# Kernel tuning notes

Hardware: AMD Instinct MI355X
Metric: run time of the kernel (lower is better)

## Reference

```python
import jax, jax.numpy as jnp
import numpy as np
from jax import lax

D_MODEL = 1024
D_IN = 1024        # expand=1 -> d_inner = d_model
N_STATE = 16       # d_state
DT_RANK = 64       # ceil(d_model/16)
D_FFN = 4096
BATCH, SEQ = 2, 2048


def setup_inputs() -> dict:
    key = jax.random.key(0)
    ks = jax.random.split(key, 12)
    r = lambda i, shape, s=0.02: jax.random.normal(ks[i], shape, jnp.float32) * s
    ones = lambda n: jnp.ones((n,), jnp.float32)
    zeros = lambda n: jnp.zeros((n,), jnp.float32)
    # S4D-real init for A
    A_log = jnp.log(jnp.tile(jnp.arange(1, N_STATE + 1, dtype=jnp.float32), (D_IN, 1)))
    return {
        "src": jax.random.normal(ks[0], (BATCH, SEQ, D_MODEL), jnp.float32),
        "in_proj_w": r(1, (2 * D_IN, D_MODEL)),
        "conv_w": r(2, (D_IN, 2), 0.5),
        "conv_b": zeros(D_IN),
        "x_proj_w": r(3, (DT_RANK + 2 * N_STATE, D_IN)),
        "dt_proj_w": r(4, (D_IN, DT_RANK), 0.1),
        "dt_proj_b": r(5, (D_IN,), 0.1),
        "A_log": A_log,
        "Dp": ones(D_IN),
        "out_proj_w": r(6, (D_MODEL, D_IN)),
        "mnorm_g": ones(D_MODEL), "mnorm_b": zeros(D_MODEL),
        "n1_g": ones(D_MODEL), "n1_b": zeros(D_MODEL),
        "n2_g": ones(D_MODEL), "n2_b": zeros(D_MODEL),
        "n3_g": ones(D_MODEL), "n3_b": zeros(D_MODEL),
        "ffn_w1": r(7, (D_FFN, D_MODEL)),
        "ffn_w2": r(8, (D_MODEL, D_FFN)),
        "fe_w": r(9, (D_MODEL, D_MODEL)),
        "fe_b": zeros(D_MODEL),
    }


def _ln(x, g, b, eps=1e-5):
    m = x.mean(-1, keepdims=True)
    v = ((x - m) ** 2).mean(-1, keepdims=True)
    return (x - m) / jnp.sqrt(v + eps) * g + b


def _mamba(x, in_proj_w, conv_w, conv_b, x_proj_w, dt_proj_w, dt_proj_b,
           A_log, Dp, out_proj_w):
    B, L, _ = x.shape
    xz = x @ in_proj_w.T                       # (B,L,2*D_IN)
    x_in, z = jnp.split(xz, 2, axis=-1)
    # depthwise causal conv1d, kernel size 2: y[l] = w0*x[l-1] + w1*x[l] + b
    x_prev = jnp.pad(x_in, ((0, 0), (1, 0), (0, 0)))[:, :L]
    x_c = jax.nn.silu(x_prev * conv_w[:, 0] + x_in * conv_w[:, 1] + conv_b)
    x_dbl = x_c @ x_proj_w.T                   # (B,L,DT_RANK+2N)
    dt, Bm, Cm = jnp.split(x_dbl, [DT_RANK, DT_RANK + N_STATE], axis=-1)
    delta = jax.nn.softplus(dt @ dt_proj_w.T + dt_proj_b)   # (B,L,D_IN)
    A = -jnp.exp(A_log)                        # (D_IN,N)
    deltaA = jnp.exp(delta[..., None] * A)                   # (B,L,D_IN,N)
    dBu = delta[..., None] * Bm[:, :, None, :] * x_c[..., None]

    def step(h, t):
        dA_t, dBu_t, C_t = t                   # (B,D_IN,N),(B,D_IN,N),(B,N)
        h = dA_t * h + dBu_t
        y = jnp.einsum('bdn,bn->bd', h, C_t)
        return h, y

    h0 = jnp.zeros((B, D_IN, N_STATE), x.dtype)
    _, ys = lax.scan(step, h0,
                     (deltaA.transpose(1, 0, 2, 3),
                      dBu.transpose(1, 0, 2, 3),
                      Cm.transpose(1, 0, 2)))
    y = ys.transpose(1, 0, 2)                  # (B,L,D_IN)
    y = (y + x_c * Dp) * jax.nn.silu(z)
    return y @ out_proj_w.T


def reference(src, in_proj_w, conv_w, conv_b, x_proj_w, dt_proj_w, dt_proj_b,
              A_log, Dp, out_proj_w, mnorm_g, mnorm_b, n1_g, n1_b, n2_g, n2_b,
              n3_g, n3_b, ffn_w1, ffn_w2, fe_w, fe_b):
    # src1 = MambaBlock(norm1(src)); dropout = identity (eval)
    h = _mamba(_ln(src, n1_g, n1_b), in_proj_w, conv_w, conv_b, x_proj_w,
               dt_proj_w, dt_proj_b, A_log, Dp, out_proj_w)
    src = src + _ln(h, mnorm_g, mnorm_b)
    # FFN: Linear -> LeakyReLU(0.01) -> Linear (no bias)
    f = _ln(src, n2_g, n2_b) @ ffn_w1.T
    f = jnp.where(f >= 0, f, 0.01 * f) @ ffn_w2.T
    src = src + f
    src = src + (_ln(src, n3_g, n3_b) @ fe_w.T + fe_b)
    return src
```

## Files before the change

### kernel.cpp

```cpp
#include <hip/hip_runtime.h>
#include <hip/hip_bf16.h>
#include <cstddef>

#define L_SEQ   2048
#define NBATCH  2
#define NROWS   (NBATCH * L_SEQ)
#define NSTATE  16
#define CH      64
#define NCHUNK  (L_SEQ / CH)

typedef __bf16 bf16x8 __attribute__((ext_vector_type(8)));
typedef float  f32x4  __attribute__((ext_vector_type(4)));
typedef unsigned short u16x4 __attribute__((ext_vector_type(4)));

static __device__ __forceinline__ unsigned short f2bf(float f) {
  unsigned int x = __builtin_bit_cast(unsigned int, f);
  x += 0x7fffu + ((x >> 16) & 1u);
  return (unsigned short)(x >> 16);
}
static __device__ __forceinline__ float bf2f(unsigned short u) {
  return __builtin_bit_cast(float, ((unsigned int)u) << 16);
}

#define GLDS(g, l) __builtin_amdgcn_global_load_lds( \
    (const __attribute__((address_space(1))) void*)(g), \
    (__attribute__((address_space(3))) void*)(l), 16, 0, 0)

#define DRAIN_VM() asm volatile("s_waitcnt vmcnt(0)" ::: "memory")

__global__ __launch_bounds__(256) void cvt_bf16_kernel(
    const float* __restrict__ in, unsigned short* __restrict__ out, int n4)
{
  const int i = blockIdx.x * 256 + threadIdx.x;
  if (i < n4) {
    const float4 v = reinterpret_cast<const float4*>(in)[i];
    u16x4 o;
    o[0] = f2bf(v.x); o[1] = f2bf(v.y); o[2] = f2bf(v.z); o[3] = f2bf(v.w);
    reinterpret_cast<u16x4*>(out)[i] = o;
  }
}

__global__ __launch_bounds__(256) void ln_kernel(
    const float* __restrict__ in, const float* __restrict__ g,
    const float* __restrict__ bta, const float* __restrict__ res,
    float* __restrict__ out, unsigned short* __restrict__ outb)
{
  const int row = blockIdx.x;
  const int tid = threadIdx.x;
  __shared__ float sm[8];
  const float4 v = reinterpret_cast<const float4*>(in + (size_t)row * 1024)[tid];
  float s = v.x + v.y + v.z + v.w;
#pragma unroll
  for (int o = 32; o > 0; o >>= 1) s += __shfl_down(s, o, 64);
  if ((tid & 63) == 0) sm[tid >> 6] = s;
  __syncthreads();
  const float mean = (sm[0] + sm[1] + sm[2] + sm[3]) * (1.f / 1024.f);
  const float dx = v.x - mean, dy = v.y - mean, dz = v.z - mean, dw = v.w - mean;
  float q = dx * dx + dy * dy + dz * dz + dw * dw;
#pragma unroll
  for (int o = 32; o > 0; o >>= 1) q += __shfl_down(q, o, 64);
  __syncthreads();
  if ((tid & 63) == 0) sm[tid >> 6] = q;
  __syncthreads();
  const float var = (sm[0] + sm[1] + sm[2] + sm[3]) * (1.f / 1024.f);
  const float rstd = rsqrtf(var + 1e-5f);
  const float4 gv = reinterpret_cast<const float4*>(g)[tid];
  const float4 bv = reinterpret_cast<const float4*>(bta)[tid];
  float4 o4;
  o4.x = dx * rstd * gv.x + bv.x;
  o4.y = dy * rstd * gv.y + bv.y;
  o4.z = dz * rstd * gv.z + bv.z;
  o4.w = dw * rstd * gv.w + bv.w;
  if (outb) {
    u16x4 ob;
    ob[0] = f2bf(o4.x); ob[1] = f2bf(o4.y); ob[2] = f2bf(o4.z); ob[3] = f2bf(o4.w);
    reinterpret_cast<u16x4*>(outb + (size_t)row * 1024)[tid] = ob;
  } else {
    if (res) {
      const float4 rv = reinterpret_cast<const float4*>(res + (size_t)row * 1024)[tid];
      o4.x += rv.x; o4.y += rv.y; o4.z += rv.z; o4.w += rv.w;
    }
    reinterpret_cast<float4*>(out + (size_t)row * 1024)[tid] = o4;
  }
}

__global__ __launch_bounds__(256) void gemm_bf16_kernel(
    const unsigned short* __restrict__ A, int lda,
    const unsigned short* __restrict__ B, int ldb,
    void* __restrict__ Cv, int ldc,
    const float* __restrict__ bias, const float* __restrict__ res,
    int K, int act, int outbf, int gy)
{
  __shared__ unsigned short As[2][128 * 32];
  __shared__ unsigned short Bs[2][128 * 32];
  const int t = threadIdx.x;
  const int w = t >> 6, l = t & 63;

  const int q = gridDim.x >> 3;
  const int nid = (blockIdx.x & 7) * q + (blockIdx.x >> 3);
  const int bm = (nid / gy) * 128;
  const int bn = (nid % gy) * 128;

  const int wr = (w >> 1) * 64, wc = (w & 1) * 64;
  f32x4 acc[4][4] = {};

  const int srow = t >> 2;
  const int sk = (t & 3) * 8;
  const unsigned short* gA0 = A + (size_t)(bm + srow) * lda + sk;
  const unsigned short* gA1 = gA0 + (size_t)64 * lda;
  const unsigned short* gB0 = B + (size_t)(bn + srow) * ldb + sk;
  const unsigned short* gB1 = gB0 + (size_t)64 * ldb;

  const int fr = l & 15;
  const int kb = (l >> 4) * 8;

#define STAGE(buf, k0) do { \
    GLDS(gA0 + (k0), &As[buf][w * 512]); \
    GLDS(gA1 + (k0), &As[buf][2048 + w * 512]); \
    GLDS(gB0 + (k0), &Bs[buf][w * 512]); \
    GLDS(gB1 + (k0), &Bs[buf][2048 + w * 512]); \
  } while (0)

#define COMPUTE(buf) do { \
    bf16x8 af[4], bfr[4]; \
    _Pragma("unroll") \
    for (int i = 0; i < 4; ++i) \
      af[i] = *reinterpret_cast<const bf16x8*>(&As[buf][(wr + i * 16 + fr) * 32 + kb]); \
    _Pragma("unroll") \
    for (int j = 0; j < 4; ++j) \
      bfr[j] = *reinterpret_cast<const bf16x8*>(&Bs[buf][(wc + j * 16 + fr) * 32 + kb]); \
    _Pragma("unroll") \
    for (int i = 0; i < 4; ++i) \
      _Pragma("unroll") \
      for (int j = 0; j < 4; ++j) \
        acc[i][j] = __builtin_amdgcn_mfma_f32_16x16x32_bf16(af[i], bfr[j], acc[i][j], 0, 0, 0); \
  } while (0)

  STAGE(0, 0);
  DRAIN_VM();
  __syncthreads();
  int cur = 0;
  for (int k0 = 32; k0 < K; k0 += 32) {
    __builtin_amdgcn_sched_barrier(0);
    STAGE(cur ^ 1, k0);
    __builtin_amdgcn_sched_barrier(0);
    COMPUTE(cur);
    DRAIN_VM();
    __syncthreads();
    cur ^= 1;
  }
  COMPUTE(cur);
#undef STAGE
#undef COMPUTE

  const int crow = (l >> 4) * 4;
  const int ccol = l & 15;
  float* Cf = (float*)Cv;
  unsigned short* Cb = (unsigned short*)Cv;
#pragma unroll
  for (int i = 0; i < 4; ++i) {
#pragma unroll
    for (int j = 0; j < 4; ++j) {
      const int n = bn + wc + j * 16 + ccol;
      const float bv = bias ? bias[n] : 0.f;
#pragma unroll
      for (int r = 0; r < 4; ++r) {
        const int m = bm + wr + i * 16 + crow + r;
        float v = acc[i][j][r] + bv;
        if (act == 1) v = (v > 20.f) ? v : __logf(1.f + __expf(v));
        else if (act == 2) v = (v >= 0.f) ? v : 0.01f * v;
        if (res) v += res[(size_t)m * ldc + n];
        if (outbf) Cb[(size_t)m * ldc + n] = f2bf(v);
        else       Cf[(size_t)m * ldc + n] = v;
      }
    }
  }
}

__global__ __launch_bounds__(256) void xproj_kernel(
    const unsigned short* __restrict__ A, int lda,
    const unsigned short* __restrict__ B, int ldb,
    float* __restrict__ C)
{
  __shared__ unsigned short As[2][128 * 32];
  __shared__ unsigned short Bs[2][96 * 32];
  const int t = threadIdx.x;
  const int w = t >> 6, l = t & 63;
  const int bm = blockIdx.x * 128;
  const int kbase = blockIdx.y * 128;

  f32x4 acc[2][6] = {};

  const int srow = t >> 2;
  const int sk = (t & 3) * 8;
  const unsigned short* gA0 = A + (size_t)(bm + srow) * lda + kbase + sk;
  const unsigned short* gA1 = gA0 + (size_t)64 * lda;
  const unsigned short* gB0 = B + (size_t)srow * ldb + kbase + sk;
  const unsigned short* gB1 = gB0 + (size_t)64 * ldb;

  const int fr = l & 15;
  const int kb = (l >> 4) * 8;

#define STAGEX(buf, k0) do { \
    GLDS(gA0 + (k0), &As[buf][w * 512]); \
    GLDS(gA1 + (k0), &As[buf][2048 + w * 512]); \
    GLDS(gB0 + (k0), &Bs[buf][w * 512]); \
    if (w < 2) GLDS(gB1 + (k0), &Bs[buf][2048 + w * 512]); \
  } while (0)

#define COMPUTEX(buf) do { \
    bf16x8 af[2], bfr[6]; \
    _Pragma("unroll") \
    for (int i = 0; i < 2; ++i) \
      af[i] = *reinterpret_cast<const bf16x8*>(&As[buf][(w * 32 + i * 16 + fr) * 32 + kb]); \
    _Pragma("unroll") \
    for (int j = 0; j < 6; ++j) \
      bfr[j] = *reinterpret_cast<const bf16x8*>(&Bs[buf][(j * 16 + fr) * 32 + kb]); \
    _Pragma("unroll") \
    for (int i = 0; i < 2; ++i) \
      _Pragma("unroll") \
      for (int j = 0; j < 6; ++j) \
        acc[i][j] = __builtin_amdgcn_mfma_f32_16x16x32_bf16(af[i], bfr[j], acc[i][j], 0, 0, 0); \
  } while (0)

  STAGEX(0, 0);
  DRAIN_VM();
  __syncthreads();
  int cur = 0;
  for (int s = 1; s < 4; ++s) {
    __builtin_amdgcn_sched_barrier(0);
    STAGEX(cur ^ 1, s * 32);
    __builtin_amdgcn_sched_barrier(0);
    COMPUTEX(cur);
    DRAIN_VM();
    __syncthreads();
    cur ^= 1;
  }
  COMPUTEX(cur);
#undef STAGEX
#undef COMPUTEX

  const int crow = (l >> 4) * 4;
  const int ccol = l & 15;
#pragma unroll
  for (int i = 0; i < 2; ++i)
#pragma unroll
    for (int j = 0; j < 6; ++j)
#pragma unroll
      for (int r = 0; r < 4; ++r) {
        const int m = bm + w * 32 + i * 16 + crow + r;
        const int n = j * 16 + ccol;
        atomicAdd(&C[(size_t)m * 96 + n], acc[i][j][r]);
      }
}

__global__ __launch_bounds__(256) void conv_silu_kernel(
    const unsigned short* __restrict__ xz, const float* __restrict__ cw,
    const float* __restrict__ cb, float* __restrict__ xc,
    unsigned short* __restrict__ xcb)
{
  const int idx = blockIdx.x * 256 + threadIdx.x;
  const int row = idx >> 10;
  const int d = idx & 1023;
  const int l = row & (L_SEQ - 1);
  const float cur = bf2f(xz[(size_t)row * 2048 + d]);
  const float prev = (l == 0) ? 0.f : bf2f(xz[(size_t)(row - 1) * 2048 + d]);
  const float v = prev * cw[d * 2 + 0] + cur * cw[d * 2 + 1] + cb[d];
  const float sv = v / (1.f + __expf(-v));
  xc[idx] = sv;
  xcb[idx] = f2bf(sv);
}

__global__ __launch_bounds__(256) void scan_pass1(
    const float* __restrict__ delta, const float* __restrict__ xc,
    const float* __restrict__ xdbl, const float* __restrict__ A_log,
    float* __restrict__ hfin, float* __restrict__ pcum)
{
  const int tid = threadIdx.x;
  const int db = blockIdx.x & 3;
  const int c = (blockIdx.x >> 2) & (NCHUNK - 1);
  const int b = blockIdx.x >> 7;
  const int d = db * 256 + tid;
  __shared__ float Bsh[CH][16];
  {
    const int lr = tid >> 2, q = tid & 3;
    const float* p = xdbl + ((size_t)(b * L_SEQ + c * CH + lr) * 96) + 64 + q * 4;
    *reinterpret_cast<float4*>(&Bsh[lr][q * 4]) = *reinterpret_cast<const float4*>(p);
  }
  float a[NSTATE];
#pragma unroll
  for (int n = 0; n < NSTATE; ++n) a[n] = -__expf(A_log[d * 16 + n]);
  __syncthreads();
  float h[NSTATE], P[NSTATE];
#pragma unroll
  for (int n = 0; n < NSTATE; ++n) { h[n] = 0.f; P[n] = 1.f; }
  const size_t rowbase = (size_t)(b * L_SEQ + c * CH);
  for (int s = 0; s < CH; ++s) {
    const size_t row = rowbase + s;
    const float dl = delta[row * 1024 + d];
    const float xcv = xc[row * 1024 + d];
#pragma unroll
    for (int n = 0; n < NSTATE; ++n) {
      const float dA = __expf(dl * a[n]);
      h[n] = h[n] * dA + (dl * Bsh[s][n]) * xcv;
      P[n] *= dA;
    }
  }
  const size_t base = ((size_t)((b * NCHUNK + c) * 1024 + d)) * 16;
  float4* hp = reinterpret_cast<float4*>(hfin + base);
  float4* pp = reinterpret_cast<float4*>(pcum + base);
#pragma unroll
  for (int qq = 0; qq < 4; ++qq) {
    hp[qq] = make_float4(h[qq * 4], h[qq * 4 + 1], h[qq * 4 + 2], h[qq * 4 + 3]);
    pp[qq] = make_float4(P[qq * 4], P[qq * 4 + 1], P[qq * 4 + 2], P[qq * 4 + 3]);
  }
}

__global__ __launch_bounds__(256) void scan_pass2(
    const float* __restrict__ hfin, const float* __restrict__ pcum,
    float* __restrict__ hstart)
{
  const int t = blockIdx.x * 256 + threadIdx.x;
  const int b = t >> 14;
  const int dn = t & 16383;
  const size_t base = (size_t)b * NCHUNK * 16384 + dn;
  float h = 0.f;
  for (int c = 0; c < NCHUNK; ++c) {
    const size_t idx = base + (size_t)c * 16384;
    hstart[idx] = h;
    h = pcum[idx] * h + hfin[idx];
  }
}

__global__ __launch_bounds__(256) void scan_pass3(
    const float* __restrict__ delta, const float* __restrict__ xc,
    const float* __restrict__ xdbl, const float* __restrict__ A_log,
    const float* __restrict__ hstart, const float* __restrict__ Dp,
    const unsigned short* __restrict__ xz, unsigned short* __restrict__ yout)
{
  const int tid = threadIdx.x;
  const int db = blockIdx.x & 3;
  const int c = (blockIdx.x >> 2) & (NCHUNK - 1);
  const int b = blockIdx.x >> 7;
  const int d = db * 256 + tid;
  __shared__ float Bsh[CH][16];
  __shared__ float Csh[CH][16];
  {
    const int lr = tid >> 2, q = tid & 3;
    const float* p = xdbl + ((size_t)(b * L_SEQ + c * CH + lr) * 96);
    *reinterpret_cast<float4*>(&Bsh[lr][q * 4]) = *reinterpret_cast<const float4*>(p + 64 + q * 4);
    *reinterpret_cast<float4*>(&Csh[lr][q * 4]) = *reinterpret_cast<const float4*>(p + 80 + q * 4);
  }
  float a[NSTATE];
#pragma unroll
  for (int n = 0; n < NSTATE; ++n) a[n] = -__expf(A_log[d * 16 + n]);
  float h[NSTATE];
  {
    const size_t base = ((size_t)((b * NCHUNK + c) * 1024 + d)) * 16;
    const float4* hp = reinterpret_cast<const float4*>(hstart + base);
#pragma unroll
    for (int qq = 0; qq < 4; ++qq) {
      const float4 v = hp[qq];
      h[qq * 4] = v.x; h[qq * 4 + 1] = v.y; h[qq * 4 + 2] = v.z; h[qq * 4 + 3] = v.w;
    }
  }
  const float dpv = Dp[d];
  __syncthreads();
  const size_t rowbase = (size_t)(b * L_SEQ + c * CH);
  for (int s = 0; s < CH; ++s) {
    const size_t row = rowbase + s;
    const float dl = delta[row * 1024 + d];
    const float xcv = xc[row * 1024 + d];
    float y = 0.f;
#pragma unroll
    for (int n = 0; n < NSTATE; ++n) {
      const float dA = __expf(dl * a[n]);
      h[n] = h[n] * dA + (dl * Bsh[s][n]) * xcv;
      y += h[n] * Csh[s][n];
    }
    const float z = bf2f(xz[row * 2048 + 1024 + d]);
    const float sil = z / (1.f + __expf(-z));
    yout[row * 1024 + d] = f2bf((y + xcv * dpv) * sil);
  }
}

extern "C" void kernel_launch(void* const* d_in, const int* in_sizes, int n_in,
                              void* d_out, int out_size, void* d_ws, size_t ws_size,
                              hipStream_t stream)
{
  (void)in_sizes; (void)n_in; (void)out_size; (void)ws_size;
  const float* src        = (const float*)d_in[0];
  const float* in_proj_w  = (const float*)d_in[1];
  const float* conv_w     = (const float*)d_in[2];
  const float* conv_b     = (const float*)d_in[3];
  const float* x_proj_w   = (const float*)d_in[4];
  const float* dt_proj_w  = (const float*)d_in[5];
  const float* dt_proj_b  = (const float*)d_in[6];
  const float* A_log      = (const float*)d_in[7];
  const float* Dp         = (const float*)d_in[8];
  const float* out_proj_w = (const float*)d_in[9];
  const float* mnorm_g    = (const float*)d_in[10];
  const float* mnorm_b    = (const float*)d_in[11];
  const float* n1_g       = (const float*)d_in[12];
  const float* n1_b       = (const float*)d_in[13];
  const float* n2_g       = (const float*)d_in[14];
  const float* n2_b       = (const float*)d_in[15];
  const float* n3_g       = (const float*)d_in[16];
  const float* n3_b       = (const float*)d_in[17];
  const float* ffn_w1     = (const float*)d_in[18];
  const float* ffn_w2     = (const float*)d_in[19];
  const float* fe_w       = (const float*)d_in[20];
  const float* fe_b       = (const float*)d_in[21];
  float* out = (float*)d_out;
  float* ws  = (float*)d_ws;

  unsigned short* xzb  = (unsigned short*)ws;
  unsigned short* xdblb= (unsigned short*)(ws + 4194304);
  unsigned short* dtwb = (unsigned short*)(ws + 4390912);
  float* xc    = ws + 8388608;
  float* xdbl  = ws + 12582912;
  float* delta = ws + 13107200;
  float* s5    = ws + 17301504;
  float* src1  = ws + 21495808;
  float* hfin  = ws + 25690112;
  float* pcum  = ws + 26738688;
  float* hst   = ws + 27787264;
  unsigned short* s1b  = (unsigned short*)(ws + 28835840);
  unsigned short* xcb  = (unsigned short*)(ws + 30932992);
  unsigned short* yb   = (unsigned short*)(ws + 33030144);
  unsigned short* f1b  = (unsigned short*)(ws + 35127296);
  unsigned short* ipwb = (unsigned short*)(ws + 43515904);
  unsigned short* xpwb = (unsigned short*)(ws + 44564480);
  unsigned short* opwb = (unsigned short*)(ws + 44613632);
  unsigned short* w1b  = (unsigned short*)(ws + 45137920);
  unsigned short* w2b  = (unsigned short*)(ws + 47235072);
  unsigned short* fewb = (unsigned short*)(ws + 49332224);

  const dim3 blk(256);

  cvt_bf16_kernel<<<2048, blk, 0, stream>>>(in_proj_w, ipwb, 524288);
  cvt_bf16_kernel<<<96,   blk, 0, stream>>>(x_proj_w, xpwb, 24576);
  cvt_bf16_kernel<<<64,   blk, 0, stream>>>(dt_proj_w, dtwb, 16384);
  cvt_bf16_kernel<<<1024, blk, 0, stream>>>(out_proj_w, opwb, 262144);
  cvt_bf16_kernel<<<4096, blk, 0, stream>>>(ffn_w1, w1b, 1048576);
  cvt_bf16_kernel<<<4096, blk, 0, stream>>>(ffn_w2, w2b, 1048576);
  cvt_bf16_kernel<<<1024, blk, 0, stream>>>(fe_w, fewb, 262144);

  ln_kernel<<<NROWS, blk, 0, stream>>>(src, n1_g, n1_b, nullptr, nullptr, s1b);
  gemm_bf16_kernel<<<512, blk, 0, stream>>>(s1b, 1024, ipwb, 1024, xzb, 2048,
                                            nullptr, nullptr, 1024, 0, 1, 16);
  conv_silu_kernel<<<16384, blk, 0, stream>>>(xzb, conv_w, conv_b, xc, xcb);
  hipMemsetAsync(xdbl, 0, (size_t)NROWS * 96 * sizeof(float), stream);
  xproj_kernel<<<dim3(32, 8), blk, 0, stream>>>(xcb, 1024, xpwb, 1024, xdbl);
  cvt_bf16_kernel<<<384, blk, 0, stream>>>(xdbl, xdblb, 98304);
  gemm_bf16_kernel<<<256, blk, 0, stream>>>(xdblb, 96, dtwb, 64, delta, 1024,
                                            dt_proj_b, nullptr, 64, 1, 0, 8);
  scan_pass1<<<256, blk, 0, stream>>>(delta, xc, xdbl, A_log, hfin, pcum);
  scan_pass2<<<128, blk, 0, stream>>>(hfin, pcum, hst);
  scan_pass3<<<256, blk, 0, stream>>>(delta, xc, xdbl, A_log, hst, Dp, xzb, yb);
  gemm_bf16_kernel<<<256, blk, 0, stream>>>(yb, 1024, opwb, 1024, s5, 1024,
                                            nullptr, nullptr, 1024, 0, 0, 8);
  ln_kernel<<<NROWS, blk, 0, stream>>>(s5, mnorm_g, mnorm_b, src, src1, nullptr);
  ln_kernel<<<NROWS, blk, 0, stream>>>(src1, n2_g, n2_b, nullptr, nullptr, s1b);
  gemm_bf16_kernel<<<1024, blk, 0, stream>>>(s1b, 1024, w1b, 1024, f1b, 4096,
                                             nullptr, nullptr, 1024, 2, 1, 32);
  gemm_bf16_kernel<<<256, blk, 0, stream>>>(f1b, 4096, w2b, 4096, s5, 1024,
                                            nullptr, src1, 4096, 0, 0, 8);
  ln_kernel<<<NROWS, blk, 0, stream>>>(s5, n3_g, n3_b, nullptr, nullptr, s1b);
  gemm_bf16_kernel<<<256, blk, 0, stream>>>(s1b, 1024, fewb, 1024, out, 1024,
                                            fe_b, s5, 1024, 0, 0, 8);
}
```

Measured before the change: 446.1 us.

## Triple-buffer GEMM LDS pipeline and merge weight conversions into one launch

The GEMM main loop moves from double to triple buffering in LDS. Loads are issued two tiles ahead and each iteration waits with a partial vmcnt, so only one barrier is needed per K-step instead of a full drain plus sync. Separately, the seven bf16 weight-conversion launches are folded into a single kernel that picks its source by index range, which cuts launch overhead. The extra buffer raises LDS use from 32KB to 48KB per block, which may lower occupancy.

```diff
diff --git a/kernel.cpp b/kernel.cpp
--- a/kernel.cpp
+++ b/kernel.cpp
@@ -38,6 +38,32 @@
     o[0] = f2bf(v.x); o[1] = f2bf(v.y); o[2] = f2bf(v.z); o[3] = f2bf(v.w);
     reinterpret_cast<u16x4*>(out)[i] = o;
   }
+}
+
+__global__ __launch_bounds__(256) void cvt_all_kernel(
+    const float* __restrict__ ipw, const float* __restrict__ xpw,
+    const float* __restrict__ dtw, const float* __restrict__ opw,
+    const float* __restrict__ w1,  const float* __restrict__ w2,
+    const float* __restrict__ few,
+    unsigned short* __restrict__ o_ipw, unsigned short* __restrict__ o_xpw,
+    unsigned short* __restrict__ o_dtw, unsigned short* __restrict__ o_opw,
+    unsigned short* __restrict__ o_w1,  unsigned short* __restrict__ o_w2,
+    unsigned short* __restrict__ o_few)
+{
+  int i = blockIdx.x * 256 + threadIdx.x;
+  const float* src; unsigned short* dst;
+  if (i < 524288)                 { src = ipw; dst = o_ipw; }
+  else if ((i -= 524288) < 24576) { src = xpw; dst = o_xpw; }
+  else if ((i -= 24576) < 16384)  { src = dtw; dst = o_dtw; }
+  else if ((i -= 16384) < 262144) { src = opw; dst = o_opw; }
+  else if ((i -= 262144) < 1048576){ src = w1; dst = o_w1; }
+  else if ((i -= 1048576) < 1048576){ src = w2; dst = o_w2; }
+  else if ((i -= 1048576) < 262144){ src = few; dst = o_few; }
+  else return;
+  const float4 v = reinterpret_cast<const float4*>(src)[i];
+  u16x4 o;
+  o[0] = f2bf(v.x); o[1] = f2bf(v.y); o[2] = f2bf(v.z); o[3] = f2bf(v.w);
+  reinterpret_cast<u16x4*>(dst)[i] = o;
 }
 
 __global__ __launch_bounds__(256) void ln_kernel(
@@ -91,8 +117,8 @@
     const float* __restrict__ bias, const float* __restrict__ res,
     int K, int act, int outbf, int gy)
 {
-  __shared__ unsigned short As[2][128 * 32];
-  __shared__ unsigned short Bs[2][128 * 32];
+  __shared__ unsigned short As[3][128 * 32];
+  __shared__ unsigned short Bs[3][128 * 32];
   const int t = threadIdx.x;
   const int w = t >> 6, l = t & 63;
 
@@ -136,20 +162,24 @@
         acc[i][j] = __builtin_amdgcn_mfma_f32_16x16x32_bf16(af[i], bfr[j], acc[i][j], 0, 0, 0); \
   } while (0)
 
+  const int nt = K >> 5;
   STAGE(0, 0);
-  DRAIN_VM();
-  __syncthreads();
-  int cur = 0;
-  for (int k0 = 32; k0 < K; k0 += 32) {
+  if (nt > 1) STAGE(1, 32);
+  int rd = 0;
+  for (int i = 0; i < nt; ++i) {
+    if (i + 1 < nt) asm volatile("s_waitcnt vmcnt(4)" ::: "memory");
+    else            asm volatile("s_waitcnt vmcnt(0)" ::: "memory");
+    __builtin_amdgcn_s_barrier();
     __builtin_amdgcn_sched_barrier(0);
-    STAGE(cur ^ 1, k0);
+    if (i + 2 < nt) {
+      const int wb = (rd + 2 >= 3) ? rd - 1 : rd + 2;
+      STAGE(wb, (i + 2) * 32);
+      __builtin_amdgcn_sched_barrier(0);
+    }
+    COMPUTE(rd);
     __builtin_amdgcn_sched_barrier(0);
-    COMPUTE(cur);
-    DRAIN_VM();
-    __syncthreads();
-    cur ^= 1;
-  }
-  COMPUTE(cur);
+    rd = (rd + 1 == 3) ? 0 : rd + 1;
+  }
 #undef STAGE
 #undef COMPUTE
 
@@ -438,13 +468,9 @@
 
   const dim3 blk(256);
 
-  cvt_bf16_kernel<<<2048, blk, 0, stream>>>(in_proj_w, ipwb, 524288);
-  cvt_bf16_kernel<<<96,   blk, 0, stream>>>(x_proj_w, xpwb, 24576);
-  cvt_bf16_kernel<<<64,   blk, 0, stream>>>(dt_proj_w, dtwb, 16384);
-  cvt_bf16_kernel<<<1024, blk, 0, stream>>>(out_proj_w, opwb, 262144);
-  cvt_bf16_kernel<<<4096, blk, 0, stream>>>(ffn_w1, w1b, 1048576);
-  cvt_bf16_kernel<<<4096, blk, 0, stream>>>(ffn_w2, w2b, 1048576);
-  cvt_bf16_kernel<<<1024, blk, 0, stream>>>(fe_w, fewb, 262144);
+  cvt_all_kernel<<<12448, blk, 0, stream>>>(
+      in_proj_w, x_proj_w, dt_proj_w, out_proj_w, ffn_w1, ffn_w2, fe_w,
+      ipwb, xpwb, dtwb, opwb, w1b, w2b, fewb);
 
   ln_kernel<<<NROWS, blk, 0, stream>>>(src, n1_g, n1_b, nullptr, nullptr, s1b);
   gemm_bf16_kernel<<<512, blk, 0, stream>>>(s1b, 1024, ipwb, 1024, xzb, 2048,
```

Result: no change. 451.2 us (+1.1%).
